# Kernel tuning notes

Measured on AMD Instinct MI355X. Metric: run time of the kernel, lower is better.

## Reference

```python
import jax, jax.numpy as jnp
import numpy as np

SIZE = 512
K = 100000.0
EPS = 1e-05


def setup_inputs() -> dict:
    key = jax.random.key(0)
    contour = jax.random.uniform(key, (128, 2), dtype=jnp.float32)
    return {"contour": contour}


def reference(contour):
    size, k, eps = SIZE, K, EPS
    # mesh: (size^2, 1, 2), normalized pixel coordinates (ij indexing like torch.meshgrid)
    coords = jnp.arange(size, dtype=jnp.float32)
    mesh = jnp.stack(jnp.meshgrid(coords, coords, indexing="ij"), axis=-1)
    mesh = mesh.reshape(-1, 1, 2) / size

    diff = contour[None, :, :] - mesh              # (P, N, 2), P = size^2
    roll_diff = jnp.roll(diff, -1, axis=1)          # next contour point
    # roll by 1 along a size-2 axis == swap (x, y)
    prod = diff * roll_diff[:, :, ::-1]             # (P, N, 2)
    sign = jnp.tanh(k * (prod[:, :, 1] - prod[:, :, 0]))  # cross-product sign

    norm_diff = jnp.linalg.norm(diff, axis=2)
    norm_roll = jnp.linalg.norm(roll_diff, axis=2)
    scalar_product = jnp.sum(diff * roll_diff, axis=2)
    cos_ang = jnp.clip(scalar_product / (norm_diff * norm_roll), -1.0 + eps, 1.0 - eps)
    angles = jnp.arccos(cos_ang)                    # (P, N)

    sum_angles = jnp.clip(jnp.sum(sign * angles, axis=1) / (2.0 * jnp.pi), 0.0, 1.0)
    return sum_angles.reshape(1, 1, size, size)
```

## Files before the change

kernel.cpp:

```cpp
#include <hip/hip_runtime.h>
#include <math.h>

#define SIZE 512
#define NPTS 128

__global__ __launch_bounds__(256) void contour_mask_kernel(
    const float* __restrict__ contour, float* __restrict__ out)
{
    __shared__ float2 c[NPTS];

    const int tid = threadIdx.x;
    if (tid < NPTS) {
        c[tid] = ((const float2*)contour)[tid];
    }
    __syncthreads();

    const int p = blockIdx.x * 256 + tid;
    const int i = p >> 9;
    const int j = p & (SIZE - 1);

    const float mx = (float)i * (1.0f / SIZE);
    const float my = (float)j * (1.0f / SIZE);

    const float K    = 100000.0f;
    const float EPS  = 1e-5f;
    const float PI_F = 3.14159265358979f;
    const float CTHR = 6e-5f;

    float ax  = c[0].x - mx;
    float ay  = c[0].y - my;
    float na2 = ax * ax + ay * ay;

    float acc = 0.0f;

    #pragma unroll 8
    for (int n = 0; n < NPTS; ++n) {
        const int n1 = (n + 1) & (NPTS - 1);
        const float2 cn = c[n1];
        const float bx  = cn.x - mx;
        const float by  = cn.y - my;
        const float nb2 = bx * bx + by * by;

        const float cross = ay * bx - ax * by;
        const float dot   = ax * bx + ay * by;

        const float inv = __builtin_amdgcn_rsqf(na2 * nb2);
        const float cosang =
            __builtin_amdgcn_fmed3f(dot * inv, -1.0f + EPS, 1.0f - EPS);

        const float xa = fabsf(cosang);
        const float t  = __builtin_amdgcn_sqrtf(1.0f - xa);
        float poly = fmaf(-0.0187293f, xa, 0.0742610f);
        poly = fmaf(poly, xa, -0.2121144f);
        poly = fmaf(poly, xa, 1.5707288f);
        const float r0  = t * poly;
        const float ang = (cosang >= 0.0f) ? r0 : (PI_F - r0);

        float s;
        if (__any(fabsf(cross) < CTHR)) {
            const float e = __expf(2.0f * K * cross);
            s = fmaf(-2.0f, __builtin_amdgcn_rcpf(e + 1.0f), 1.0f);
        } else {
            s = copysignf(1.0f, cross);
        }

        acc = fmaf(s, ang, acc);

        ax = bx; ay = by; na2 = nb2;
    }

    float r = acc * (1.0f / (2.0f * PI_F));
    r = fminf(fmaxf(r, 0.0f), 1.0f);
    out[p] = r;
}

extern "C" void kernel_launch(void* const* d_in, const int* in_sizes, int n_in,
                              void* d_out, int out_size, void* d_ws, size_t ws_size,
                              hipStream_t stream) {
    const float* contour = (const float*)d_in[0];
    float* out = (float*)d_out;

    const int total = SIZE * SIZE;
    const int block = 256;
    const int grid  = total / block;

    contour_mask_kernel<<<grid, block, 0, stream>>>(contour, out);
}
```

Before: 77.88 us.

## Compute angle via atan2 polynomial and process two pixels per thread

```diff
diff --git a/kernel.cpp b/kernel.cpp
--- a/kernel.cpp
+++ b/kernel.cpp
@@ -15,63 +15,87 @@
     }
     __syncthreads();
 
-    const int p = blockIdx.x * 256 + tid;
-    const int i = p >> 9;
-    const int j = p & (SIZE - 1);
+    const int i  = blockIdx.x;
+    const int j0 = tid;
+    const int j1 = tid + 256;
+    const int p0 = i * SIZE + j0;
+    const int p1 = i * SIZE + j1;
 
-    const float mx = (float)i * (1.0f / SIZE);
-    const float my = (float)j * (1.0f / SIZE);
+    const float mx  = (float)i  * (1.0f / SIZE);
+    const float my0 = (float)j0 * (1.0f / SIZE);
+    const float my1 = (float)j1 * (1.0f / SIZE);
 
     const float K    = 100000.0f;
-    const float EPS  = 1e-5f;
     const float PI_F = 3.14159265358979f;
+    const float HPI  = 1.57079632679490f;
+    const float ANG_LO = 4.4721397e-3f;
+    const float ANG_HI = 3.1371205f;
     const float CTHR = 6e-5f;
 
     float ax  = c[0].x - mx;
-    float ay  = c[0].y - my;
-    float na2 = ax * ax + ay * ay;
+    float ay0 = c[0].y - my0;
+    float ay1 = c[0].y - my1;
 
-    float acc = 0.0f;
+    float acc0 = 0.0f, acc1 = 0.0f;
 
-    #pragma unroll 8
+    #pragma unroll 4
     for (int n = 0; n < NPTS; ++n) {
         const int n1 = (n + 1) & (NPTS - 1);
         const float2 cn = c[n1];
         const float bx  = cn.x - mx;
-        const float by  = cn.y - my;
-        const float nb2 = bx * bx + by * by;
+        const float by0 = cn.y - my0;
+        const float by1 = cn.y - my1;
 
-        const float cross = ay * bx - ax * by;
-        const float dot   = ax * bx + ay * by;
+        const float cr0 = fmaf(ay0, bx, -ax * by0);
+        const float dt0 = fmaf(ax,  bx,  ay0 * by0);
+        const float cr1 = fmaf(ay1, bx, -ax * by1);
+        const float dt1 = fmaf(ax,  bx,  ay1 * by1);
 
-        const float inv = __builtin_amdgcn_rsqf(na2 * nb2);
-        const float cosang =
-            __builtin_amdgcn_fmed3f(dot * inv, -1.0f + EPS, 1.0f - EPS);
+        const float ac0 = fabsf(cr0), ad0 = fabsf(dt0);
+        const float ac1 = fabsf(cr1), ad1 = fabsf(dt1);
+        const float mn0 = fminf(ac0, ad0), mx0_ = fmaxf(ac0, ad0);
+        const float mn1 = fminf(ac1, ad1), mx1_ = fmaxf(ac1, ad1);
+        const float t0 = mn0 * __builtin_amdgcn_rcpf(mx0_);
+        const float t1 = mn1 * __builtin_amdgcn_rcpf(mx1_);
+        const float s0 = t0 * t0;
+        const float s1 = t1 * t1;
 
-        const float xa = fabsf(cosang);
-        const float t  = __builtin_amdgcn_sqrtf(1.0f - xa);
-        float poly = fmaf(-0.0187293f, xa, 0.0742610f);
-        poly = fmaf(poly, xa, -0.2121144f);
-        poly = fmaf(poly, xa, 1.5707288f);
-        const float r0  = t * poly;
-        const float ang = (cosang >= 0.0f) ? r0 : (PI_F - r0);
+        float q0 = fmaf(-0.01172120f, s0, 0.05265332f);
+        float q1 = fmaf(-0.01172120f, s1, 0.05265332f);
+        q0 = fmaf(q0, s0, -0.11643287f);  q1 = fmaf(q1, s1, -0.11643287f);
+        q0 = fmaf(q0, s0,  0.19354346f);  q1 = fmaf(q1, s1,  0.19354346f);
+        q0 = fmaf(q0, s0, -0.33262347f);  q1 = fmaf(q1, s1, -0.33262347f);
+        q0 = fmaf(q0, s0,  0.99997726f);  q1 = fmaf(q1, s1,  0.99997726f);
+        float a0 = t0 * q0;
+        float a1 = t1 * q1;
 
-        float s;
-        if (__any(fabsf(cross) < CTHR)) {
-            const float e = __expf(2.0f * K * cross);
-            s = fmaf(-2.0f, __builtin_amdgcn_rcpf(e + 1.0f), 1.0f);
+        a0 = (ac0 > ad0) ? (HPI - a0) : a0;
+        a1 = (ac1 > ad1) ? (HPI - a1) : a1;
+        a0 = (dt0 < 0.0f) ? (PI_F - a0) : a0;
+        a1 = (dt1 < 0.0f) ? (PI_F - a1) : a1;
+
+        a0 = __builtin_amdgcn_fmed3f(a0, ANG_LO, ANG_HI);
+        a1 = __builtin_amdgcn_fmed3f(a1, ANG_LO, ANG_HI);
+
+        if (__any(fminf(ac0, ac1) < CTHR)) {
+            const float e0 = __expf(2.0f * K * cr0);
+            const float e1 = __expf(2.0f * K * cr1);
+            const float sg0 = fmaf(-2.0f, __builtin_amdgcn_rcpf(e0 + 1.0f), 1.0f);
+            const float sg1 = fmaf(-2.0f, __builtin_amdgcn_rcpf(e1 + 1.0f), 1.0f);
+            acc0 = fmaf(sg0, a0, acc0);
+            acc1 = fmaf(sg1, a1, acc1);
         } else {
-            s = copysignf(1.0f, cross);
+            acc0 += __builtin_copysignf(a0, cr0);
+            acc1 += __builtin_copysignf(a1, cr1);
         }
 
-        acc = fmaf(s, ang, acc);
-
-        ax = bx; ay = by; na2 = nb2;
+        ax = bx; ay0 = by0; ay1 = by1;
     }
 
-    float r = acc * (1.0f / (2.0f * PI_F));
-    r = fminf(fmaxf(r, 0.0f), 1.0f);
-    out[p] = r;
+    float r0 = acc0 * (1.0f / (2.0f * PI_F));
+    float r1 = acc1 * (1.0f / (2.0f * PI_F));
+    out[p0] = __builtin_amdgcn_fmed3f(r0, 0.0f, 1.0f);
+    out[p1] = __builtin_amdgcn_fmed3f(r1, 0.0f, 1.0f);
 }
 
 extern "C" void kernel_launch(void* const* d_in, const int* in_sizes, int n_in,
@@ -80,9 +104,8 @@
     const float* contour = (const float*)d_in[0];
     float* out = (float*)d_out;
 
-    const int total = SIZE * SIZE;
     const int block = 256;
-    const int grid  = total / block;
+    const int grid  = SIZE;
 
     contour_mask_kernel<<<grid, block, 0, stream>>>(contour, out);
 }
```

After: 77.89 us. Within noise of the previous version (+0.0%).
